# Optimization experiments

Hardware: AMD Instinct MI355X
Metric: run time of the kernel (lower is better)

The kernel has to match this reference:

```python
import jax, jax.numpy as jnp
import numpy as np

N, K, D = 100000, 16, 128

def setup_inputs() -> dict:
    key = jax.random.key(0)
    k1, k2, k3, k4, k5 = jax.random.split(key, 5)
    s = 1.0 / np.sqrt(D)  # nn.Linear default init scale
    return {
        "h": jax.random.normal(k1, (N, D), dtype=jnp.float32),
        "nbr_idx": jax.random.randint(k2, (N, K), 0, N, dtype=jnp.int64),
        "nbr_w": jax.random.uniform(k3, (N, K), dtype=jnp.float32),
        "w_self": jax.random.uniform(k4, (D, D), minval=-s, maxval=s, dtype=jnp.float32),
        "w_nei": jax.random.uniform(k5, (D, D), minval=-s, maxval=s, dtype=jnp.float32),
        "ln_gamma": jnp.ones((D,), dtype=jnp.float32),
        "ln_beta": jnp.zeros((D,), dtype=jnp.float32),
    }

def layer_norm(x, gamma, beta, eps=1e-5):
    mu = jnp.mean(x, axis=-1, keepdims=True)
    var = jnp.mean(jnp.square(x - mu), axis=-1, keepdims=True)
    return (x - mu) * jax.lax.rsqrt(var + eps) * gamma + beta

def reference(h, nbr_idx, nbr_w, w_self, w_nei, ln_gamma, ln_beta):
    # gather neighbor features: [N, K, D]
    nei = h[nbr_idx]
    # weighted sum over neighbors -> [N, D]
    agg = jnp.einsum('nk,nkd->nd', nbr_w, nei)
    # dual linear (nn.Linear applies x @ W.T) + exact (erf) GELU
    out = jax.nn.gelu(h @ w_self.T + agg @ w_nei.T, approximate=False)
    # dropout is identity at inference; then LayerNorm
    return layer_norm(out, ln_gamma, ln_beta)
```

## Files before the change

kernel.cpp:

```cpp
#include <hip/hip_runtime.h>
#include <hip/hip_bf16.h>
#include <math.h>

#define DFEAT 128
#define KNBR  16
#define NPB   64

typedef __attribute__((ext_vector_type(8))) short short8;
typedef __attribute__((ext_vector_type(4))) float f32x4;

__device__ __forceinline__ unsigned short f2bf(float x) {
    union { float f; unsigned u; } v; v.f = x;
    unsigned r = v.u + 0x7FFFu + ((v.u >> 16) & 1u);
    return (unsigned short)(r >> 16);
}
__device__ __forceinline__ float bf2f(unsigned short u) {
    union { unsigned u; float f; } v; v.u = ((unsigned)u) << 16; return v.f;
}

__global__ __launch_bounds__(256)
void prep_kernel(const float* __restrict__ h,
                 const float* __restrict__ wself,
                 const float* __restrict__ wnei,
                 unsigned short* __restrict__ h16,
                 unsigned short* __restrict__ wcat,
                 int ntot8) {
    const int t = blockIdx.x * 256 + threadIdx.x;
    if (t < 4096) {
        const int base = t * 8;
        const int j = base >> 8;
        const int d0 = base & 255;
        const float* src = (d0 < DFEAT) ? (wself + j * DFEAT + d0)
                                        : (wnei  + j * DFEAT + (d0 - DFEAT));
        f32x4 a = ((const f32x4*)src)[0], b = ((const f32x4*)src)[1];
        short8 o;
        o[0] = f2bf(a[0]); o[1] = f2bf(a[1]); o[2] = f2bf(a[2]); o[3] = f2bf(a[3]);
        o[4] = f2bf(b[0]); o[5] = f2bf(b[1]); o[6] = f2bf(b[2]); o[7] = f2bf(b[3]);
        *(short8*)(wcat + base) = o;
        return;
    }
    const long u = (long)t - 4096;
    if (u >= ntot8) return;
    f32x4 a = __builtin_nontemporal_load((const f32x4*)(h + u * 8));
    f32x4 b = __builtin_nontemporal_load((const f32x4*)(h + u * 8) + 1);
    short8 o;
    o[0] = f2bf(a[0]); o[1] = f2bf(a[1]); o[2] = f2bf(a[2]); o[3] = f2bf(a[3]);
    o[4] = f2bf(b[0]); o[5] = f2bf(b[1]); o[6] = f2bf(b[2]); o[7] = f2bf(b[3]);
    __builtin_nontemporal_store(o, (short8*)(h16 + u * 8));
}

template<int H16>
__global__ __launch_bounds__(256, 4)
void sage_fused_kernel(const float* __restrict__ h,
                       const unsigned short* __restrict__ h16,
                       const int* __restrict__ nbr32,
                       const float* __restrict__ nbrw,
                       const unsigned short* __restrict__ wcat,
                       const float* __restrict__ gamma,
                       const float* __restrict__ beta,
                       float* __restrict__ out,
                       int N) {
    __shared__ __align__(16) unsigned short xlds[NPB][256];

    const int tid = threadIdx.x;
    const int nb  = blockIdx.x * NPB;

    const bool idx64 = ((nbr32[1] | nbr32[3] | nbr32[5] | nbr32[7] |
                         nbr32[9] | nbr32[11] | nbr32[13] | nbr32[15]) == 0);

    const int l   = tid & 63;
    const int wvi = tid >> 6;
    const int q   = l & 15;
    const int gb  = l & 48;
    const int i0  = wvi * 16 + (l >> 4) * 4;

    if constexpr (H16) {
        int   nn[4]; int myidx[4]; float myw[4]; short8 hv[4];
        #pragma unroll
        for (int r = 0; r < 4; ++r) {
            int n = nb + i0 + r; if (n >= N) n = N - 1;
            nn[r] = n;
            const int e = n * KNBR + q;
            myidx[r] = __builtin_nontemporal_load(&nbr32[idx64 ? 2 * e : e]);
            myw[r]   = __builtin_nontemporal_load(&nbrw[e]);
        }
        #pragma unroll
        for (int r = 0; r < 4; ++r)
            hv[r] = *(const short8*)(h16 + (long)nn[r] * DFEAT + q * 8);

        short8 bufA[8], bufB[8];
        float  acc[8];

        #define ISSUE(BUF, r, hh)                                             \
            _Pragma("unroll")                                                 \
            for (int k8 = 0; k8 < 8; ++k8) {                                  \
                int ik = __shfl(myidx[r], gb + (hh) * 8 + k8, 64);            \
                BUF[k8] = *(const short8*)(h16 + (long)ik * DFEAT + q * 8);   \
            }
        #define CONSUME(BUF, r, hh)                                           \
            _Pragma("unroll")                                                 \
            for (int k8 = 0; k8 < 8; ++k8) {                                  \
                float wk = __shfl(myw[r], gb + (hh) * 8 + k8, 64);            \
                _Pragma("unroll")                                             \
                for (int d = 0; d < 8; ++d)                                   \
                    acc[d] += wk * bf2f((unsigned short)BUF[k8][d]);          \
            }
        #define RESET() { _Pragma("unroll") for (int d = 0; d < 8; ++d) acc[d] = 0.f; }
        #define STORE(r) {                                                    \
            const int i = i0 + (r);                                           \
            *(short8*)&xlds[i][(q ^ (i & 7)) * 8] = hv[r];                    \
            short8 ab;                                                        \
            _Pragma("unroll") for (int d = 0; d < 8; ++d) ab[d] = f2bf(acc[d]); \
            *(short8*)&xlds[i][((16 + q) ^ (i & 7)) * 8] = ab; }

        ISSUE(bufA, 0, 0); ISSUE(bufB, 0, 1);
        RESET(); CONSUME(bufA, 0, 0); ISSUE(bufA, 1, 0);
                 CONSUME(bufB, 0, 1); ISSUE(bufB, 1, 1); STORE(0);
        RESET(); CONSUME(bufA, 1, 0); ISSUE(bufA, 2, 0);
                 CONSUME(bufB, 1, 1); ISSUE(bufB, 2, 1); STORE(1);
        RESET(); CONSUME(bufA, 2, 0); ISSUE(bufA, 3, 0);
                 CONSUME(bufB, 2, 1); ISSUE(bufB, 3, 1); STORE(2);
        RESET(); CONSUME(bufA, 3, 0);
                 CONSUME(bufB, 3, 1); STORE(3);
        #undef ISSUE
        #undef CONSUME
        #undef RESET
        #undef STORE
    } else {
        #pragma unroll 1
        for (int r = 0; r < 4; ++r) {
            const int i = i0 + r;
            int n = nb + i; if (n >= N) n = N - 1;
            short8 hv;
            float acc[8] = {0.f,0.f,0.f,0.f,0.f,0.f,0.f,0.f};
            const f32x4* hrow = (const f32x4*)(h + (long)n * DFEAT + q * 8);
            f32x4 h0 = hrow[0], h1 = hrow[1];
            hv[0] = f2bf(h0[0]); hv[1] = f2bf(h0[1]); hv[2] = f2bf(h0[2]); hv[3] = f2bf(h0[3]);
            hv[4] = f2bf(h1[0]); hv[5] = f2bf(h1[1]); hv[6] = f2bf(h1[2]); hv[7] = f2bf(h1[3]);
            const int e0 = n * KNBR;
            #pragma unroll 4
            for (int k = 0; k < KNBR; ++k) {
                float w = nbrw[e0 + k];
                int idx = nbr32[idx64 ? 2 * (e0 + k) : (e0 + k)];
                const f32x4* nrow = (const f32x4*)(h + (long)idx * DFEAT + q * 8);
                f32x4 n0 = nrow[0], n1 = nrow[1];
                acc[0] += w * n0[0]; acc[1] += w * n0[1];
                acc[2] += w * n0[2]; acc[3] += w * n0[3];
                acc[4] += w * n1[0]; acc[5] += w * n1[1];
                acc[6] += w * n1[2]; acc[7] += w * n1[3];
            }
            *(short8*)&xlds[i][(q ^ (i & 7)) * 8] = hv;
            short8 ab;
            #pragma unroll
            for (int d = 0; d < 8; ++d) ab[d] = f2bf(acc[d]);
            *(short8*)&xlds[i][((16 + q) ^ (i & 7)) * 8] = ab;
        }
    }
    __syncthreads();

    const int wv  = wvi;
    const int col = l & 15;
    const int kg  = l >> 4;

    f32x4 acc2[4][2];
    #pragma unroll
    for (int s = 0; s < 4; ++s)
        #pragma unroll
        for (int t = 0; t < 2; ++t)
            acc2[s][t] = (f32x4){0.f, 0.f, 0.f, 0.f};

    const unsigned short* wbase0 = wcat + (wv * 32 + col) * 256 + kg * 8;
    const unsigned short* wbase1 = wbase0 + 16 * 256;

    #pragma unroll
    for (int kk = 0; kk < 8; ++kk) {
        short8 b0 = *(const short8*)(wbase0 + kk * 32);
        short8 b1 = *(const short8*)(wbase1 + kk * 32);
        #pragma unroll
        for (int s = 0; s < 4; ++s) {
            const int row = s * 16 + col;
            const int c = (kk * 4 + kg) ^ (row & 7);
            short8 a = *(const short8*)&xlds[row][c * 8];
            acc2[s][0] = __builtin_amdgcn_mfma_f32_16x16x32_bf16(a, b0, acc2[s][0], 0, 0, 0);
            acc2[s][1] = __builtin_amdgcn_mfma_f32_16x16x32_bf16(a, b1, acc2[s][1], 0, 0, 0);
        }
    }

    float y[4][2][4];
    #pragma unroll
    for (int s = 0; s < 4; ++s)
        #pragma unroll
        for (int t = 0; t < 2; ++t)
            #pragma unroll
            for (int r = 0; r < 4; ++r) {
                float x = acc2[s][t][r];
                y[s][t][r] = 0.5f * x * (1.0f + erff(x * 0.70710678118654752f));
            }

    __syncthreads();

    float* lsum = (float*)&xlds[0][0];
    float* lsq  = lsum + 4 * NPB;

    #pragma unroll
    for (int s = 0; s < 4; ++s) {
        f32x4 sm, sq;
        #pragma unroll
        for (int r = 0; r < 4; ++r) {
            float a0 = y[s][0][r], a1 = y[s][1][r];
            sm[r] = a0 + a1;
            sq[r] = a0 * a0 + a1 * a1;
        }
        #pragma unroll
        for (int m = 1; m < 16; m <<= 1) {
            #pragma unroll
            for (int r = 0; r < 4; ++r) {
                sm[r] += __shfl_xor(sm[r], m, 64);
                sq[r] += __shfl_xor(sq[r], m, 64);
            }
        }
        if (col == 0) {
            *(f32x4*)&lsum[wv * NPB + s * 16 + kg * 4] = sm;
            *(f32x4*)&lsq [wv * NPB + s * 16 + kg * 4] = sq;
        }
    }
    __syncthreads();

    const float g0  = gamma[wv * 32 + col];
    const float g1  = gamma[wv * 32 + 16 + col];
    const float be0 = beta [wv * 32 + col];
    const float be1 = beta [wv * 32 + 16 + col];

    #pragma unroll
    for (int s = 0; s < 4; ++s) {
        f32x4 sm = {0.f,0.f,0.f,0.f}, sq = {0.f,0.f,0.f,0.f};
        #pragma unroll
        for (int u = 0; u < 4; ++u) {
            f32x4 a = *(const f32x4*)&lsum[u * NPB + s * 16 + kg * 4];
            f32x4 b = *(const f32x4*)&lsq [u * NPB + s * 16 + kg * 4];
            sm += a; sq += b;
        }
        #pragma unroll
        for (int r = 0; r < 4; ++r) {
            const int i = s * 16 + kg * 4 + r;
            const int n = nb + i;
            if (n < N) {
                float mean = sm[r] * (1.0f / 128.0f);
                float var  = sq[r] * (1.0f / 128.0f) - mean * mean;
                float rstd = rsqrtf(var + 1e-5f);
                long o = (long)n * DFEAT + wv * 32 + col;
                __builtin_nontemporal_store((y[s][0][r] - mean) * rstd * g0 + be0, &out[o]);
                __builtin_nontemporal_store((y[s][1][r] - mean) * rstd * g1 + be1, &out[o + 16]);
            }
        }
    }
}

extern "C" void kernel_launch(void* const* d_in, const int* in_sizes, int n_in,
                              void* d_out, int out_size, void* d_ws, size_t ws_size,
                              hipStream_t stream) {
    const float* h     = (const float*)d_in[0];
    const int*   nbr   = (const int*)  d_in[1];
    const float* nbrw  = (const float*)d_in[2];
    const float* wself = (const float*)d_in[3];
    const float* wnei  = (const float*)d_in[4];
    const float* gamma = (const float*)d_in[5];
    const float* beta  = (const float*)d_in[6];
    const int N = in_sizes[0] / DFEAT;

    unsigned short* wcat = (unsigned short*)d_ws;
    unsigned short* h16  = (unsigned short*)((char*)d_ws + 65536);
    const size_t need = 65536 + (size_t)N * DFEAT * sizeof(unsigned short);

    const int blocks = (N + NPB - 1) / NPB;
    if (ws_size >= need) {
        const int ntot8 = N * DFEAT / 8;
        const int pthreads = 4096 + ntot8;
        prep_kernel<<<(pthreads + 255) / 256, 256, 0, stream>>>(h, wself, wnei, h16, wcat, ntot8);
        sage_fused_kernel<1><<<blocks, 256, 0, stream>>>(h, h16, nbr, nbrw, wcat,
                                                         gamma, beta, (float*)d_out, N);
    } else {
        prep_kernel<<<(4096 + 255) / 256, 256, 0, stream>>>(h, wself, wnei, h16, wcat, 0);
        sage_fused_kernel<0><<<blocks, 256, 0, stream>>>(h, (const unsigned short*)nullptr,
                                                         nbr, nbrw, wcat,
                                                         gamma, beta, (float*)d_out, N);
    }
}
```

Measured before the change: 94.52 us.

## Gather neighbor features from per-row int8 quantized copy with row scales

The prep kernel now also writes an int8 copy of h with one absmax scale per row. A new fused-kernel mode gathers neighbor rows from this int8 copy, folding each row's scale into its edge weight, so each gathered row costs half the bytes of the bf16 copy. Each lane now handles 16 features and two rows instead of 8 features and four rows. The change adds a byte-per-element write in prep, drops the earlier explicit double-buffered prefetch, and lowers aggregation precision to 8 bits, which may exceed tolerance.

```diff
diff --git a/kernel.cpp b/kernel.cpp
--- a/kernel.cpp
+++ b/kernel.cpp
@@ -8,6 +8,8 @@
 
 typedef __attribute__((ext_vector_type(8))) short short8;
 typedef __attribute__((ext_vector_type(4))) float f32x4;
+typedef __attribute__((ext_vector_type(2))) unsigned u32x2;
+typedef __attribute__((ext_vector_type(4))) unsigned u32x4;
 
 __device__ __forceinline__ unsigned short f2bf(float x) {
     union { float f; unsigned u; } v; v.f = x;
@@ -24,6 +26,8 @@
                  const float* __restrict__ wnei,
                  unsigned short* __restrict__ h16,
                  unsigned short* __restrict__ wcat,
+                 unsigned char* __restrict__ h8i,
+                 float* __restrict__ sc,
                  int ntot8) {
     const int t = blockIdx.x * 256 + threadIdx.x;
     if (t < 4096) {
@@ -47,12 +51,34 @@
     o[0] = f2bf(a[0]); o[1] = f2bf(a[1]); o[2] = f2bf(a[2]); o[3] = f2bf(a[3]);
     o[4] = f2bf(b[0]); o[5] = f2bf(b[1]); o[6] = f2bf(b[2]); o[7] = f2bf(b[3]);
     __builtin_nontemporal_store(o, (short8*)(h16 + u * 8));
-}
-
-template<int H16>
+
+    if (h8i) {
+        float m = 0.f;
+        #pragma unroll
+        for (int d = 0; d < 4; ++d) { m = fmaxf(m, fabsf(a[d])); m = fmaxf(m, fabsf(b[d])); }
+        #pragma unroll
+        for (int mk = 1; mk < 16; mk <<= 1) m = fmaxf(m, __shfl_xor(m, mk, 64));
+        const float inv = (m > 0.f) ? 127.f / m : 0.f;
+        u32x2 q;
+        q[0] = ((unsigned)((int)rintf(a[0] * inv) & 255))
+             | ((unsigned)((int)rintf(a[1] * inv) & 255) << 8)
+             | ((unsigned)((int)rintf(a[2] * inv) & 255) << 16)
+             | ((unsigned)((int)rintf(a[3] * inv) & 255) << 24);
+        q[1] = ((unsigned)((int)rintf(b[0] * inv) & 255))
+             | ((unsigned)((int)rintf(b[1] * inv) & 255) << 8)
+             | ((unsigned)((int)rintf(b[2] * inv) & 255) << 16)
+             | ((unsigned)((int)rintf(b[3] * inv) & 255) << 24);
+        __builtin_nontemporal_store(q, (u32x2*)(h8i + u * 8));
+        if ((u & 15) == 0) sc[u >> 4] = m * (1.f / 127.f);
+    }
+}
+
+template<int MODE>
 __global__ __launch_bounds__(256, 4)
 void sage_fused_kernel(const float* __restrict__ h,
                        const unsigned short* __restrict__ h16,
+                       const unsigned char* __restrict__ h8i,
+                       const float* __restrict__ sc,
                        const int* __restrict__ nbr32,
                        const float* __restrict__ nbrw,
                        const unsigned short* __restrict__ wcat,
@@ -70,63 +96,84 @@
 
     const int l   = tid & 63;
     const int wvi = tid >> 6;
-    const int q   = l & 15;
-    const int gb  = l & 48;
-    const int i0  = wvi * 16 + (l >> 4) * 4;
-
-    if constexpr (H16) {
-        int   nn[4]; int myidx[4]; float myw[4]; short8 hv[4];
-        #pragma unroll
+
+    if constexpr (MODE == 3) {
+        const int q8  = l & 7;
+        const int gb2 = l & 56;
+        const int i0b = wvi * 16 + (l >> 3) * 2;
+
+        #pragma unroll
+        for (int r = 0; r < 2; ++r) {
+            const int i = i0b + r;
+            int n = nb + i; if (n >= N) n = N - 1;
+
+            const int e0 = n * KNBR + q8;
+            const int id0 = nbr32[idx64 ? 2 * e0 : e0];
+            const int id1 = nbr32[idx64 ? 2 * (e0 + 8) : (e0 + 8)];
+            const float w0 = nbrw[e0]     * sc[id0];
+            const float w1 = nbrw[e0 + 8] * sc[id1];
+
+            short8 hv0 = *(const short8*)(h16 + (long)n * DFEAT + q8 * 16);
+            short8 hv1 = *(const short8*)(h16 + (long)n * DFEAT + q8 * 16 + 8);
+            *(short8*)&xlds[i][((2 * q8)     ^ (i & 7)) * 8] = hv0;
+            *(short8*)&xlds[i][((2 * q8 + 1) ^ (i & 7)) * 8] = hv1;
+
+            float acc[16];
+            #pragma unroll
+            for (int d = 0; d < 16; ++d) acc[d] = 0.f;
+
+            #pragma unroll
+            for (int k = 0; k < 16; ++k) {
+                const int   ik = __shfl(k < 8 ? id0 : id1, gb2 + (k & 7), 64);
+                const float wk = __shfl(k < 8 ? w0  : w1,  gb2 + (k & 7), 64);
+                u32x4 nv = *(const u32x4*)(h8i + (long)ik * DFEAT + q8 * 16);
+                #pragma unroll
+                for (int b = 0; b < 4; ++b) {
+                    const unsigned u = nv[b];
+                    acc[b * 4 + 0] += wk * (float)(signed char)(u & 0xFF);
+                    acc[b * 4 + 1] += wk * (float)(signed char)((u >> 8) & 0xFF);
+                    acc[b * 4 + 2] += wk * (float)(signed char)((u >> 16) & 0xFF);
+                    acc[b * 4 + 3] += wk * (float)(signed char)(u >> 24);
+                }
+            }
+
+            short8 ab0, ab1;
+            #pragma unroll
+            for (int d = 0; d < 8; ++d) { ab0[d] = f2bf(acc[d]); ab1[d] = f2bf(acc[8 + d]); }
+            *(short8*)&xlds[i][((16 + 2 * q8)     ^ (i & 7)) * 8] = ab0;
+            *(short8*)&xlds[i][((16 + 2 * q8 + 1) ^ (i & 7)) * 8] = ab1;
+        }
+    } else if constexpr (MODE == 1) {
+        const int q  = l & 15;
+        const int gb = l & 48;
+        const int i0 = wvi * 16 + (l >> 4) * 4;
+        #pragma unroll 1
         for (int r = 0; r < 4; ++r) {
-            int n = nb + i0 + r; if (n >= N) n = N - 1;
-            nn[r] = n;
-            const int e = n * KNBR + q;
-            myidx[r] = __builtin_nontemporal_load(&nbr32[idx64 ? 2 * e : e]);
-            myw[r]   = __builtin_nontemporal_load(&nbrw[e]);
-        }
-        #pragma unroll
-        for (int r = 0; r < 4; ++r)
-            hv[r] = *(const short8*)(h16 + (long)nn[r] * DFEAT + q * 8);
-
-        short8 bufA[8], bufB[8];
-        float  acc[8];
-
-        #define ISSUE(BUF, r, hh)                                             \
-            _Pragma("unroll")                                                 \
-            for (int k8 = 0; k8 < 8; ++k8) {                                  \
-                int ik = __shfl(myidx[r], gb + (hh) * 8 + k8, 64);            \
-                BUF[k8] = *(const short8*)(h16 + (long)ik * DFEAT + q * 8);   \
-            }
-        #define CONSUME(BUF, r, hh)                                           \
-            _Pragma("unroll")                                                 \
-            for (int k8 = 0; k8 < 8; ++k8) {                                  \
-                float wk = __shfl(myw[r], gb + (hh) * 8 + k8, 64);            \
-                _Pragma("unroll")                                             \
-                for (int d = 0; d < 8; ++d)                                   \
-                    acc[d] += wk * bf2f((unsigned short)BUF[k8][d]);          \
-            }
-        #define RESET() { _Pragma("unroll") for (int d = 0; d < 8; ++d) acc[d] = 0.f; }
-        #define STORE(r) {                                                    \
-            const int i = i0 + (r);                                           \
-            *(short8*)&xlds[i][(q ^ (i & 7)) * 8] = hv[r];                    \
-            short8 ab;                                                        \
-            _Pragma("unroll") for (int d = 0; d < 8; ++d) ab[d] = f2bf(acc[d]); \
-            *(short8*)&xlds[i][((16 + q) ^ (i & 7)) * 8] = ab; }
-
-        ISSUE(bufA, 0, 0); ISSUE(bufB, 0, 1);
-        RESET(); CONSUME(bufA, 0, 0); ISSUE(bufA, 1, 0);
-                 CONSUME(bufB, 0, 1); ISSUE(bufB, 1, 1); STORE(0);
-        RESET(); CONSUME(bufA, 1, 0); ISSUE(bufA, 2, 0);
-                 CONSUME(bufB, 1, 1); ISSUE(bufB, 2, 1); STORE(1);
-        RESET(); CONSUME(bufA, 2, 0); ISSUE(bufA, 3, 0);
-                 CONSUME(bufB, 2, 1); ISSUE(bufB, 3, 1); STORE(2);
-        RESET(); CONSUME(bufA, 3, 0);
-                 CONSUME(bufB, 3, 1); STORE(3);
-        #undef ISSUE
-        #undef CONSUME
-        #undef RESET
-        #undef STORE
+            const int i = i0 + r;
+            int n = nb + i; if (n >= N) n = N - 1;
+            const int e0 = n * KNBR + q;
+            int myidx = nbr32[idx64 ? 2 * e0 : e0];
+            float myw = nbrw[e0];
+            short8 hv = *(const short8*)(h16 + (long)n * DFEAT + q * 8);
+            float acc[8] = {0.f,0.f,0.f,0.f,0.f,0.f,0.f,0.f};
+            #pragma unroll
+            for (int k = 0; k < KNBR; ++k) {
+                int ik = __shfl(myidx, gb + k, 64);
+                short8 nv = *(const short8*)(h16 + (long)ik * DFEAT + q * 8);
+                float wk = __shfl(myw, gb + k, 64);
+                #pragma unroll
+                for (int d = 0; d < 8; ++d)
+                    acc[d] += wk * bf2f((unsigned short)nv[d]);
+            }
+            *(short8*)&xlds[i][(q ^ (i & 7)) * 8] = hv;
+            short8 ab;
+            #pragma unroll
+            for (int d = 0; d < 8; ++d) ab[d] = f2bf(acc[d]);
+            *(short8*)&xlds[i][((16 + q) ^ (i & 7)) * 8] = ab;
+        }
     } else {
+        const int q  = l & 15;
+        const int i0 = wvi * 16 + (l >> 4) * 4;
         #pragma unroll 1
         for (int r = 0; r < 4; ++r) {
             const int i = i0 + r;
@@ -270,19 +317,31 @@
 
     unsigned short* wcat = (unsigned short*)d_ws;
     unsigned short* h16  = (unsigned short*)((char*)d_ws + 65536);
-    const size_t need = 65536 + (size_t)N * DFEAT * sizeof(unsigned short);
+    float*          sc   = (float*)((char*)d_ws + 65536 + (size_t)N * DFEAT * 2);
+    unsigned char*  h8i  = (unsigned char*)((char*)sc + (size_t)N * 4);
+    const size_t need16 = 65536 + (size_t)N * DFEAT * 2;
+    const size_t need3  = need16 + (size_t)N * 4 + (size_t)N * DFEAT;
 
     const int blocks = (N + NPB - 1) / NPB;
-    if (ws_size >= need) {
-        const int ntot8 = N * DFEAT / 8;
-        const int pthreads = 4096 + ntot8;
-        prep_kernel<<<(pthreads + 255) / 256, 256, 0, stream>>>(h, wself, wnei, h16, wcat, ntot8);
-        sage_fused_kernel<1><<<blocks, 256, 0, stream>>>(h, h16, nbr, nbrw, wcat,
+    const int ntot8 = N * DFEAT / 8;
+    const int pthreads = 4096 + ntot8;
+
+    if (ws_size >= need3) {
+        prep_kernel<<<(pthreads + 255) / 256, 256, 0, stream>>>(h, wself, wnei, h16, wcat, h8i, sc, ntot8);
+        sage_fused_kernel<3><<<blocks, 256, 0, stream>>>(h, h16, h8i, sc, nbr, nbrw, wcat,
+                                                         gamma, beta, (float*)d_out, N);
+    } else if (ws_size >= need16) {
+        prep_kernel<<<(pthreads + 255) / 256, 256, 0, stream>>>(h, wself, wnei, h16, wcat,
+                                                                (unsigned char*)nullptr, (float*)nullptr, ntot8);
+        sage_fused_kernel<1><<<blocks, 256, 0, stream>>>(h, h16, (const unsigned char*)nullptr,
+                                                         (const float*)nullptr, nbr, nbrw, wcat,
                                                          gamma, beta, (float*)d_out, N);
     } else {
-        prep_kernel<<<(4096 + 255) / 256, 256, 0, stream>>>(h, wself, wnei, h16, wcat, 0);
+        prep_kernel<<<(4096 + 255) / 256, 256, 0, stream>>>(h, wself, wnei, h16, wcat,
+                                                            (unsigned char*)nullptr, (float*)nullptr, 0);
         sage_fused_kernel<0><<<blocks, 256, 0, stream>>>(h, (const unsigned short*)nullptr,
-                                                         nbr, nbrw, wcat,
+                                                         (const unsigned char*)nullptr,
+                                                         (const float*)nullptr, nbr, nbrw, wcat,
                                                          gamma, beta, (float*)d_out, N);
     }
 }
```

Measured after the change: 85.92 us (median of 2 runs). -9.1%, faster.
